# Optimization experiments

Hardware: AMD Instinct MI355X
Metric: run time of the kernel (lower is better)

The kernel has to match this reference:

```python
import jax, jax.numpy as jnp
import numpy as np

N = 2_000_000

# HydroParam bounds in order [S1max, ks, n]
_LOWS = np.array([100.0, 0.01, 0.01], dtype=np.float32)
_HIGHS = np.array([500.0, 100.0, 10.0], dtype=np.float32)


def setup_inputs() -> dict:
    key = jax.random.key(0)
    ks = jax.random.split(key, 8)
    x = jax.random.normal(ks[0], (N, 4), dtype=jnp.float32)
    S1 = jax.random.uniform(ks[1], (N, 1), dtype=jnp.float32)  # nonnegative storage
    # Three identical MLPs (S1max, ks, n) stacked on leading axis k=3
    W1 = jax.random.normal(ks[2], (3, 4, 6), dtype=jnp.float32) * 0.5
    b1 = jax.random.normal(ks[3], (3, 6), dtype=jnp.float32) * 0.1
    W2 = jax.random.normal(ks[4], (3, 6, 6), dtype=jnp.float32) * 0.5
    b2 = jax.random.normal(ks[5], (3, 6), dtype=jnp.float32) * 0.1
    W3 = jax.random.normal(ks[6], (3, 6, 1), dtype=jnp.float32) * 0.5
    b3 = jax.random.normal(ks[7], (3, 1), dtype=jnp.float32) * 0.1
    return {"x": x, "S1": S1, "W1": W1, "b1": b1, "W2": W2, "b2": b2, "W3": W3, "b3": b3}


def reference(x, S1, W1, b1, W2, b2, W3, b3):
    # Batched tiny MLP: k=3 params, N rows, widths 4->6->6->1, tanh hidden acts
    h = jnp.tanh(jnp.einsum('nd,kdw->knw', x, W1) + b1[:, None, :])   # [3,N,6]
    h = jnp.tanh(jnp.einsum('knw,kwv->knv', h, W2) + b2[:, None, :])  # [3,N,6]
    y = jnp.einsum('knv,kvo->kno', h, W3) + b3[:, None, :]            # [3,N,1]
    lows = jnp.asarray(_LOWS)[:, None, None]
    ranges = jnp.asarray(_HIGHS - _LOWS)[:, None, None]
    vals = ranges * jax.nn.sigmoid(y) + lows                           # HydroParam affine-sigmoid
    S1max_val, ks_val, n_val = vals[0], vals[1], vals[2]               # each [N,1]
    subsurf_flow = ks_val * (S1 / S1max_val) ** n_val
    return jnp.clip(subsurf_flow, 0.0, S1max_val)
```

## Files before the change

### kernel.cpp

```cpp
#include <hip/hip_runtime.h>

#if __has_builtin(__builtin_amdgcn_exp2f)
#define FAST_EXP2(x) __builtin_amdgcn_exp2f(x)
#else
#define FAST_EXP2(x) exp2f(x)
#endif
#if __has_builtin(__builtin_amdgcn_logf)
#define FAST_LOG2(x) __builtin_amdgcn_logf(x)
#else
#define FAST_LOG2(x) log2f(x)
#endif
#if __has_builtin(__builtin_amdgcn_rcpf)
#define FAST_RCP(x) __builtin_amdgcn_rcpf(x)
#else
#define FAST_RCP(x) (1.0f / (x))
#endif

#define LOG2E 1.44269504088896340736f

typedef float v2f __attribute__((ext_vector_type(2)));

__device__ __forceinline__ v2f v2fma(v2f a, v2f b, v2f c) {
    return __builtin_elementwise_fma(a, b, c);
}

__device__ __forceinline__ v2f fast_tanh2(v2f v) {
    v2f t = v * (v2f)(2.0f * LOG2E);
    v2f e;
    e.x = FAST_EXP2(t.x);
    e.y = FAST_EXP2(t.y);
    v2f d = e + (v2f)(1.0f);
    v2f r;
    r.x = FAST_RCP(d.x);
    r.y = FAST_RCP(d.y);
    return v2fma((v2f)(-2.0f), r, (v2f)(1.0f));
}

__device__ __forceinline__ float fast_sigmoid(float v) {
    return FAST_RCP(1.0f + FAST_EXP2(-v * LOG2E));
}

#define ROWS 4

__global__ __launch_bounds__(256) void subsurf_kernel(
    const float* __restrict__ x, const float* __restrict__ S1,
    const float* __restrict__ W1, const float* __restrict__ b1,
    const float* __restrict__ W2, const float* __restrict__ b2,
    const float* __restrict__ W3, const float* __restrict__ b3,
    float* __restrict__ out, int n)
{
    __shared__ __align__(16) float w[240];
    int t = threadIdx.x;
    if (t < 72)       w[t] = W1[t];
    else if (t < 90)  w[t] = b1[t - 72];
    else if (t < 198) w[t] = W2[t - 90];
    else if (t < 216) w[t] = b2[t - 198];
    else if (t < 234) w[t] = W3[t - 216];
    else if (t < 237) w[t] = b3[t - 234];
    __syncthreads();

    const v2f* W1p = (const v2f*)(w + 0);
    const v2f* b1p = (const v2f*)(w + 72);
    const v2f* W2p = (const v2f*)(w + 90);
    const v2f* b2p = (const v2f*)(w + 198);
    const float* W3s = w + 216;
    const float* b3s = w + 234;

    const float lows[3]   = {100.0f, 0.01f, 0.01f};
    const float ranges[3] = {500.0f - 100.0f, 100.0f - 0.01f, 10.0f - 0.01f};

    int base = blockIdx.x * (256 * ROWS) + t;

    int i_cur = base < n ? base : (n - 1);
    float4 xv = ((const float4*)x)[i_cur];
    float s1 = S1[i_cur];

    #pragma unroll
    for (int j = 0; j < ROWS; ++j) {
        int i = base + j * 256;
        float4 xv_n;
        float s1_n = 0.0f;
        if (j + 1 < ROWS) {
            int i_next = (i + 256) < n ? (i + 256) : (n > 0 ? n - 1 : 0);
            xv_n = ((const float4*)x)[i_next];
            s1_n = S1[i_next];
        }

        float xs[4] = {xv.x, xv.y, xv.z, xv.w};

        float vals[3];
        #pragma unroll
        for (int k = 0; k < 3; ++k) {
            float h1[6];
            #pragma unroll
            for (int jp = 0; jp < 3; ++jp) {
                v2f acc = b1p[k * 3 + jp];
                #pragma unroll
                for (int d = 0; d < 4; ++d)
                    acc = v2fma((v2f)(xs[d]), W1p[(k * 4 + d) * 3 + jp], acc);
                v2f th = fast_tanh2(acc);
                h1[2 * jp]     = th.x;
                h1[2 * jp + 1] = th.y;
            }
            float h2[6];
            #pragma unroll
            for (int jp = 0; jp < 3; ++jp) {
                v2f acc = b2p[k * 3 + jp];
                #pragma unroll
                for (int ww = 0; ww < 6; ++ww)
                    acc = v2fma((v2f)(h1[ww]), W2p[(k * 6 + ww) * 3 + jp], acc);
                v2f th = fast_tanh2(acc);
                h2[2 * jp]     = th.x;
                h2[2 * jp + 1] = th.y;
            }
            float y = b3s[k];
            #pragma unroll
            for (int v = 0; v < 6; ++v)
                y = fmaf(h2[v], W3s[k * 6 + v], y);
            vals[k] = fmaf(ranges[k], fast_sigmoid(y), lows[k]);
        }

        float S1max = vals[0], ks = vals[1], nexp = vals[2];
        float lr = FAST_LOG2(s1) - FAST_LOG2(S1max);
        float flow = ks * FAST_EXP2(nexp * lr);
        flow = fminf(fmaxf(flow, 0.0f), S1max);
        if (i < n) out[i] = flow;

        xv = xv_n;
        s1 = s1_n;
    }
}

extern "C" void kernel_launch(void* const* d_in, const int* in_sizes, int n_in,
                              void* d_out, int out_size, void* d_ws, size_t ws_size,
                              hipStream_t stream) {
    const float* x  = (const float*)d_in[0];
    const float* S1 = (const float*)d_in[1];
    const float* W1 = (const float*)d_in[2];
    const float* b1 = (const float*)d_in[3];
    const float* W2 = (const float*)d_in[4];
    const float* b2 = (const float*)d_in[5];
    const float* W3 = (const float*)d_in[6];
    const float* b3 = (const float*)d_in[7];
    float* out = (float*)d_out;

    int n = out_size;
    int rows_per_block = 256 * ROWS;
    int grid = (n + rows_per_block - 1) / rows_per_block;
    subsurf_kernel<<<grid, 256, 0, stream>>>(x, S1, W1, b1, W2, b2, W3, b3, out, n);
}
```

Baseline: 108.3 us.

## Hoist per-MLP weights into registers and loop MLPs outside rows

Reorders the computation so the outer loop runs over the three MLPs (not unrolled) and the inner loop over the four rows. Each MLP's weights are loaded once from shared memory into registers, and the shared-memory layout is regrouped into per-MLP slices of 80 floats. All row inputs are loaded up front rather than software-pipelined one row ahead. The aim is to cut repeated LDS reads of weights per row; the cost is more VGPRs for the weight registers and the per-row intermediate arrays, and a dynamic k loop with selects, which may indirectly index the p_ arrays.

```diff
diff --git a/kernel.cpp b/kernel.cpp
--- a/kernel.cpp
+++ b/kernel.cpp
@@ -51,53 +51,75 @@
 {
     __shared__ __align__(16) float w[240];
     int t = threadIdx.x;
-    if (t < 72)       w[t] = W1[t];
-    else if (t < 90)  w[t] = b1[t - 72];
-    else if (t < 198) w[t] = W2[t - 90];
-    else if (t < 216) w[t] = b2[t - 198];
-    else if (t < 234) w[t] = W3[t - 216];
-    else if (t < 237) w[t] = b3[t - 234];
+    if (t < 240) {
+        int slice = t / 80;
+        int r = t - slice * 80;
+        float v = 0.0f;
+        if (r < 24)      v = W1[slice * 24 + r];
+        else if (r < 60) v = W2[slice * 36 + (r - 24)];
+        else if (r < 66) v = W3[slice * 6 + (r - 60)];
+        else if (r < 72) v = b1[slice * 6 + (r - 66)];
+        else if (r < 78) v = b2[slice * 6 + (r - 72)];
+        else if (r < 79) v = b3[slice];
+        w[t] = v;
+    }
     __syncthreads();
-
-    const v2f* W1p = (const v2f*)(w + 0);
-    const v2f* b1p = (const v2f*)(w + 72);
-    const v2f* W2p = (const v2f*)(w + 90);
-    const v2f* b2p = (const v2f*)(w + 198);
-    const float* W3s = w + 216;
-    const float* b3s = w + 234;
-
-    const float lows[3]   = {100.0f, 0.01f, 0.01f};
-    const float ranges[3] = {500.0f - 100.0f, 100.0f - 0.01f, 10.0f - 0.01f};
 
     int base = blockIdx.x * (256 * ROWS) + t;
 
-    int i_cur = base < n ? base : (n - 1);
-    float4 xv = ((const float4*)x)[i_cur];
-    float s1 = S1[i_cur];
-
+    float4 xv[ROWS];
+    float s1v[ROWS];
     #pragma unroll
     for (int j = 0; j < ROWS; ++j) {
         int i = base + j * 256;
-        float4 xv_n;
-        float s1_n = 0.0f;
-        if (j + 1 < ROWS) {
-            int i_next = (i + 256) < n ? (i + 256) : (n > 0 ? n - 1 : 0);
-            xv_n = ((const float4*)x)[i_next];
-            s1_n = S1[i_next];
-        }
+        int ic = i < n ? i : (n - 1);
+        xv[j] = ((const float4*)x)[ic];
+        s1v[j] = S1[ic];
+    }
 
-        float xs[4] = {xv.x, xv.y, xv.z, xv.w};
+    float p_S1max[ROWS], p_ks[ROWS], p_n[ROWS];
 
-        float vals[3];
+    #pragma unroll 1
+    for (int k = 0; k < 3; ++k) {
+        const float* s = w + k * 80;
+        const v2f* w1p = (const v2f*)(s);
+        const v2f* w2p = (const v2f*)(s + 24);
+        const v2f* w3p = (const v2f*)(s + 60);
+        const v2f* b1p = (const v2f*)(s + 66);
+        const v2f* b2p = (const v2f*)(s + 72);
+
+        v2f w1r[12];
         #pragma unroll
-        for (int k = 0; k < 3; ++k) {
+        for (int q = 0; q < 12; ++q) w1r[q] = w1p[q];
+        v2f w2r[18];
+        #pragma unroll
+        for (int q = 0; q < 18; ++q) w2r[q] = w2p[q];
+        v2f w3v[3];
+        #pragma unroll
+        for (int q = 0; q < 3; ++q) w3v[q] = w3p[q];
+        v2f b1r[3];
+        #pragma unroll
+        for (int q = 0; q < 3; ++q) b1r[q] = b1p[q];
+        v2f b2r[3];
+        #pragma unroll
+        for (int q = 0; q < 3; ++q) b2r[q] = b2p[q];
+        float b3k = s[78];
+
+        float low_k   = (k == 0) ? 100.0f : 0.01f;
+        float range_k = (k == 0) ? (500.0f - 100.0f)
+                                 : ((k == 1) ? (100.0f - 0.01f) : (10.0f - 0.01f));
+
+        #pragma unroll
+        for (int j = 0; j < ROWS; ++j) {
+            float xs[4] = {xv[j].x, xv[j].y, xv[j].z, xv[j].w};
+
             float h1[6];
             #pragma unroll
             for (int jp = 0; jp < 3; ++jp) {
-                v2f acc = b1p[k * 3 + jp];
+                v2f acc = b1r[jp];
                 #pragma unroll
                 for (int d = 0; d < 4; ++d)
-                    acc = v2fma((v2f)(xs[d]), W1p[(k * 4 + d) * 3 + jp], acc);
+                    acc = v2fma((v2f)(xs[d]), w1r[d * 3 + jp], acc);
                 v2f th = fast_tanh2(acc);
                 h1[2 * jp]     = th.x;
                 h1[2 * jp + 1] = th.y;
@@ -105,29 +127,37 @@
             float h2[6];
             #pragma unroll
             for (int jp = 0; jp < 3; ++jp) {
-                v2f acc = b2p[k * 3 + jp];
+                v2f acc = b2r[jp];
                 #pragma unroll
                 for (int ww = 0; ww < 6; ++ww)
-                    acc = v2fma((v2f)(h1[ww]), W2p[(k * 6 + ww) * 3 + jp], acc);
+                    acc = v2fma((v2f)(h1[ww]), w2r[ww * 3 + jp], acc);
                 v2f th = fast_tanh2(acc);
                 h2[2 * jp]     = th.x;
                 h2[2 * jp + 1] = th.y;
             }
-            float y = b3s[k];
-            #pragma unroll
-            for (int v = 0; v < 6; ++v)
-                y = fmaf(h2[v], W3s[k * 6 + v], y);
-            vals[k] = fmaf(ranges[k], fast_sigmoid(y), lows[k]);
+            float y = b3k;
+            y = fmaf(h2[0], w3v[0].x, y);
+            y = fmaf(h2[1], w3v[0].y, y);
+            y = fmaf(h2[2], w3v[1].x, y);
+            y = fmaf(h2[3], w3v[1].y, y);
+            y = fmaf(h2[4], w3v[2].x, y);
+            y = fmaf(h2[5], w3v[2].y, y);
+            float val = fmaf(range_k, fast_sigmoid(y), low_k);
+
+            if (k == 0)      p_S1max[j] = val;
+            else if (k == 1) p_ks[j]    = val;
+            else             p_n[j]     = val;
         }
+    }
 
-        float S1max = vals[0], ks = vals[1], nexp = vals[2];
-        float lr = FAST_LOG2(s1) - FAST_LOG2(S1max);
+    #pragma unroll
+    for (int j = 0; j < ROWS; ++j) {
+        int i = base + j * 256;
+        float S1max = p_S1max[j], ks = p_ks[j], nexp = p_n[j];
+        float lr = FAST_LOG2(s1v[j]) - FAST_LOG2(S1max);
         float flow = ks * FAST_EXP2(nexp * lr);
         flow = fminf(fmaxf(flow, 0.0f), S1max);
         if (i < n) out[i] = flow;
-
-        xv = xv_n;
-        s1 = s1_n;
     }
 }
 
```

Result: no change. 109.3 us (+0.9%).
